# Performance work log

Measured on AMD Instinct MI355X. Metric: run time of the kernel, lower is better.

Reference implementation:

```python
import jax, jax.numpy as jnp
import numpy as np

EPS = 1e-10


def setup_inputs() -> dict:
    key = jax.random.key(0)
    k1, k2 = jax.random.split(key)
    inputs = jax.random.normal(k1, (32, 64, 64, 64), dtype=jnp.float32)
    # tf.random_uniform_initializer() default: U(-0.05, 0.05)
    embeddings = jax.random.uniform(k2, (1024, 64), dtype=jnp.float32,
                                    minval=-0.05, maxval=0.05)
    return {"inputs": inputs, "embeddings": embeddings}


def reference(inputs, embeddings):
    beta = 0.25
    K, D = embeddings.shape
    input_shape = inputs.shape
    flat = inputs.reshape(-1, D)                      # [N, D]

    # squared L2 distances: |a|^2 - 2 a.b + |b|^2  -> [N, K]
    a_sq = jnp.sum(flat * flat, axis=1, keepdims=True)
    ab = 2.0 * (flat @ embeddings.T)
    b_sq = jnp.sum(embeddings * embeddings, axis=1)[None, :]
    distances = a_sq - ab + b_sq

    idx = jnp.argmin(distances, axis=1)               # [N]
    # gather nearest codes (equivalent to one_hot @ embeddings)
    quantized = embeddings[idx].reshape(input_shape)

    commitment_loss = jnp.mean(jnp.square(jax.lax.stop_gradient(quantized) - inputs))
    codebook_loss = jnp.mean(jnp.square(quantized - jax.lax.stop_gradient(inputs)))
    vq_loss = commitment_loss + beta * codebook_loss

    # straight-through estimator
    quantized_st = inputs + jax.lax.stop_gradient(quantized - inputs)

    # perplexity from code usage histogram (== mean of one-hot rows)
    N = flat.shape[0]
    counts = jnp.zeros((K,), dtype=jnp.float32).at[idx].add(1.0)
    avg_probs = counts / N
    perplexity = jnp.exp(-jnp.sum(avg_probs * jnp.log(avg_probs + EPS)))

    indices_reshaped = idx.reshape(input_shape[:-1])
    return quantized_st, indices_reshaped, perplexity, vq_loss
```

## Files before the change

### kernel.cpp

```cpp
#include <hip/hip_runtime.h>
#include <float.h>

#define N_ROWS 131072
#define DIM 64
#define KCODES 1024
#define TAU 1.0e-3f
#define FLAGBIT 0x200000
#define NBLOCKA (N_ROWS / 128)
#define NBLOCKF (N_ROWS * 4 / 256)
#define NWAVES_FIN (N_ROWS * 4 / 64)

typedef __attribute__((ext_vector_type(8))) short short8;
typedef __attribute__((ext_vector_type(4))) float f32x4;

__device__ __forceinline__ unsigned short f2bf_rne(float x) {
    unsigned int u = __float_as_uint(x);
    unsigned int r = u + 0x7FFFu + ((u >> 16) & 1u);
    return (unsigned short)(r >> 16);
}
__device__ __forceinline__ float bf2f(unsigned short h) {
    return __uint_as_float(((unsigned int)h) << 16);
}

__device__ __forceinline__ float np_pairwise_sq64(const float* v) {
    float r[8];
#pragma unroll
    for (int j = 0; j < 8; ++j) r[j] = __fmul_rn(v[j], v[j]);
#pragma unroll
    for (int i = 8; i < 64; i += 8)
#pragma unroll
        for (int j = 0; j < 8; ++j)
            r[j] = __fadd_rn(r[j], __fmul_rn(v[i + j], v[i + j]));
    return __fadd_rn(
        __fadd_rn(__fadd_rn(r[0], r[1]), __fadd_rn(r[2], r[3])),
        __fadd_rn(__fadd_rn(r[4], r[5]), __fadd_rn(r[6], r[7])));
}

__device__ __forceinline__ float np_sq_stream(const float* xr) {
    float r[8];
    {
        float4 a = *reinterpret_cast<const float4*>(xr);
        float4 b = *reinterpret_cast<const float4*>(xr + 4);
        r[0] = __fmul_rn(a.x, a.x); r[1] = __fmul_rn(a.y, a.y);
        r[2] = __fmul_rn(a.z, a.z); r[3] = __fmul_rn(a.w, a.w);
        r[4] = __fmul_rn(b.x, b.x); r[5] = __fmul_rn(b.y, b.y);
        r[6] = __fmul_rn(b.z, b.z); r[7] = __fmul_rn(b.w, b.w);
    }
#pragma unroll
    for (int i = 8; i < 64; i += 8) {
        float4 a = *reinterpret_cast<const float4*>(xr + i);
        float4 b = *reinterpret_cast<const float4*>(xr + i + 4);
        r[0] = __fadd_rn(r[0], __fmul_rn(a.x, a.x));
        r[1] = __fadd_rn(r[1], __fmul_rn(a.y, a.y));
        r[2] = __fadd_rn(r[2], __fmul_rn(a.z, a.z));
        r[3] = __fadd_rn(r[3], __fmul_rn(a.w, a.w));
        r[4] = __fadd_rn(r[4], __fmul_rn(b.x, b.x));
        r[5] = __fadd_rn(r[5], __fmul_rn(b.y, b.y));
        r[6] = __fadd_rn(r[6], __fmul_rn(b.z, b.z));
        r[7] = __fadd_rn(r[7], __fmul_rn(b.w, b.w));
    }
    return __fadd_rn(
        __fadd_rn(__fadd_rn(r[0], r[1]), __fadd_rn(r[2], r[3])),
        __fadd_rn(__fadd_rn(r[4], r[5]), __fadd_rn(r[6], r[7])));
}

__device__ __forceinline__ float np_dist_stream(const float* xr, const float* e,
                                                float a_sq, float bq) {
    double acc0 = 0.0, acc1 = 0.0, acc2 = 0.0, acc3 = 0.0;
#pragma unroll
    for (int d = 0; d < DIM; d += 4) {
        float4 ev = *reinterpret_cast<const float4*>(e + d);
        float4 xv = *reinterpret_cast<const float4*>(xr + d);
        acc0 = fma((double)xv.x, (double)ev.x, acc0);
        acc1 = fma((double)xv.y, (double)ev.y, acc1);
        acc2 = fma((double)xv.z, (double)ev.z, acc2);
        acc3 = fma((double)xv.w, (double)ev.w, acc3);
    }
    double dot = (acc0 + acc1) + (acc2 + acc3);
    float ab = (float)(2.0 * dot);
    return __fadd_rn(__fsub_rn(a_sq, ab), bq);
}

__global__ __launch_bounds__(256, 4)
void vq_prep(const float* __restrict__ emb,
             int* __restrict__ hist,
             float* __restrict__ bsqf,
             unsigned short* __restrict__ epack) {
    const int tid = blockIdx.x * 256 + threadIdx.x;
    const int c   = tid >> 4;
    const int sub = tid & 15;
    const int g   = sub & 7;
    const int lvl = sub >> 3;

    const float* e8 = emb + (size_t)c * DIM + g * 8;
    float4 v0 = *reinterpret_cast<const float4*>(e8);
    float4 v1 = *reinterpret_cast<const float4*>(e8 + 4);
    float ev[8] = {v0.x, v0.y, v0.z, v0.w, v1.x, v1.y, v1.z, v1.w};
    short8 outv;
#pragma unroll
    for (int j = 0; j < 8; ++j) {
        unsigned short hh = f2bf_rne(ev[j]);
        outv[j] = (lvl == 0) ? (short)hh : (short)f2bf_rne(ev[j] - bf2f(hh));
    }
    const size_t base =
        ((((size_t)(c >> 4) * 2 + lvl) * 2 + (g >> 2)) * 64 +
         (((g & 3) << 4) | (c & 15))) * 8;
    *reinterpret_cast<short8*>(epack + base) = outv;

    if (sub == 0) {
        float e[DIM];
        const float4* src = reinterpret_cast<const float4*>(emb + (size_t)c * DIM);
#pragma unroll
        for (int i = 0; i < DIM / 4; ++i) {
            float4 v = src[i];
            e[i * 4 + 0] = v.x; e[i * 4 + 1] = v.y;
            e[i * 4 + 2] = v.z; e[i * 4 + 3] = v.w;
        }
        bsqf[c] = np_pairwise_sq64(e);
        hist[c] = 0;
    }
}

__global__ __launch_bounds__(256, 4)
void vq_fast(const float* __restrict__ x,
             const unsigned short* __restrict__ epack,
             const float* __restrict__ bsqf,
             float* __restrict__ idxout) {
    __shared__ unsigned short lds[16384];
    __shared__ float bql[KCODES];

    const int t = threadIdx.x;
    const int lane = t & 63;
    const int wid = t >> 6;
    const int rowbase = blockIdx.x * 128 + wid * 32;
    const int arow = lane & 15;
    const int kgrp = lane >> 4;

#pragma unroll
    for (int i = 0; i < 4; ++i) bql[t + i * 256] = bsqf[t + i * 256];

    short8 ah[2][2], al[2][2];
#pragma unroll
    for (int mf = 0; mf < 2; ++mf) {
#pragma unroll
        for (int kt = 0; kt < 2; ++kt) {
            const float* src = x + (size_t)(rowbase + mf * 16 + arow) * DIM + kt * 32 + kgrp * 8;
            float4 v0 = *reinterpret_cast<const float4*>(src);
            float4 v1 = *reinterpret_cast<const float4*>(src + 4);
            float xv[8] = {v0.x, v0.y, v0.z, v0.w, v1.x, v1.y, v1.z, v1.w};
            short8 h, l;
#pragma unroll
            for (int j = 0; j < 8; ++j) {
                unsigned short hh = f2bf_rne(xv[j]);
                h[j] = (short)hh;
                l[j] = (short)f2bf_rne(xv[j] - bf2f(hh));
            }
            ah[mf][kt] = h;
            al[mf][kt] = l;
        }
    }

    float best[2][4], sec[2][4];
    int bidx[2][4], sidx[2][4];
#pragma unroll
    for (int mf = 0; mf < 2; ++mf)
#pragma unroll
        for (int r = 0; r < 4; ++r) {
            best[mf][r] = FLT_MAX; sec[mf][r] = FLT_MAX;
            bidx[mf][r] = 0; sidx[mf][r] = 0;
        }

    for (int ch = 0; ch < 8; ++ch) {
        __syncthreads();
        {
            const float4* gsrc = reinterpret_cast<const float4*>(epack + (size_t)ch * 16384);
            float4* ldst = reinterpret_cast<float4*>(lds);
#pragma unroll
            for (int i = 0; i < 8; ++i)
                ldst[t + i * 256] = gsrc[t + i * 256];
        }
        __syncthreads();

        for (int ctl = 0; ctl < 8; ++ctl) {
            const int code0 = (ch * 8 + ctl) * 16;
            const unsigned short* fb = lds + ctl * 2048 + lane * 8;
            short8 bh0 = *reinterpret_cast<const short8*>(fb + 0 * 512);
            short8 bh1 = *reinterpret_cast<const short8*>(fb + 1 * 512);
            short8 bl0 = *reinterpret_cast<const short8*>(fb + 2 * 512);
            short8 bl1 = *reinterpret_cast<const short8*>(fb + 3 * 512);
            const float bq = bql[code0 + arow];

            f32x4 acc[2];
#pragma unroll
            for (int mf = 0; mf < 2; ++mf) {
                f32x4 a = {0.f, 0.f, 0.f, 0.f};
                a = __builtin_amdgcn_mfma_f32_16x16x32_bf16(ah[mf][0], bh0, a, 0, 0, 0);
                a = __builtin_amdgcn_mfma_f32_16x16x32_bf16(ah[mf][1], bh1, a, 0, 0, 0);
                a = __builtin_amdgcn_mfma_f32_16x16x32_bf16(ah[mf][0], bl0, a, 0, 0, 0);
                a = __builtin_amdgcn_mfma_f32_16x16x32_bf16(ah[mf][1], bl1, a, 0, 0, 0);
                a = __builtin_amdgcn_mfma_f32_16x16x32_bf16(al[mf][0], bh0, a, 0, 0, 0);
                a = __builtin_amdgcn_mfma_f32_16x16x32_bf16(al[mf][1], bh1, a, 0, 0, 0);
                acc[mf] = a;
            }

            const int code = code0 + arow;
#pragma unroll
            for (int mf = 0; mf < 2; ++mf)
#pragma unroll
                for (int r = 0; r < 4; ++r) {
                    float s = fmaf(-2.0f, acc[mf][r], bq);
                    bool lt_b = s < best[mf][r];
                    bool lt_s = s < sec[mf][r];
                    sec[mf][r]  = lt_b ? best[mf][r] : (lt_s ? s : sec[mf][r]);
                    sidx[mf][r] = lt_b ? bidx[mf][r] : (lt_s ? code : sidx[mf][r]);
                    best[mf][r] = lt_b ? s : best[mf][r];
                    bidx[mf][r] = lt_b ? code : bidx[mf][r];
                }
        }
    }

#pragma unroll
    for (int mf = 0; mf < 2; ++mf)
#pragma unroll
        for (int r = 0; r < 4; ++r) {
            float b = best[mf][r], sc = sec[mf][r];
            int bi = bidx[mf][r], si = sidx[mf][r];
#pragma unroll
            for (int off = 1; off < 16; off <<= 1) {
                float ob  = __shfl_xor(b, off);
                int   obi = __shfl_xor(bi, off);
                float osc = __shfl_xor(sc, off);
                int   osi = __shfl_xor(si, off);
                bool o_lt = ob < b;
                float loser  = o_lt ? b  : ob;
                int   loseri = o_lt ? bi : obi;
                b  = o_lt ? ob  : b;
                bi = o_lt ? obi : bi;
                float ns = sc; int nsi = si;
                if (osc < ns)   { ns = osc;   nsi = osi; }
                if (loser < ns) { ns = loser; nsi = loseri; }
                sc = ns; si = nsi;
            }
            best[mf][r] = b; sec[mf][r] = sc;
            bidx[mf][r] = bi; sidx[mf][r] = si;
        }

    if ((lane & 15) == 0) {
        const int rgrp = lane >> 4;
#pragma unroll
        for (int mf = 0; mf < 2; ++mf)
#pragma unroll
            for (int r = 0; r < 4; ++r) {
                int row = rowbase + mf * 16 + rgrp * 4 + r;
                int bi = bidx[mf][r], si = sidx[mf][r];
                int lo = min(bi, si), hi = max(bi, si);
                bool flag = (sec[mf][r] - best[mf][r]) <= TAU;
                int enc = flag ? (FLAGBIT | lo | (hi << 10)) : bi;
                idxout[row] = (float)enc;
            }
    }
}

__global__ __launch_bounds__(256, 8)
void vq_finalize(const float* __restrict__ x,
                 const float* __restrict__ emb,
                 const float* __restrict__ bsqf,
                 float* __restrict__ idxout,
                 float* __restrict__ qout,
                 int* __restrict__ hist,
                 float* __restrict__ partials) {
    const int gid  = blockIdx.x * 256 + threadIdx.x;
    const int row  = gid >> 2;
    const int part = gid & 3;
    int v = (int)idxout[row];
    int k;
    if (v & FLAGBIT) {
        const int c1 = v & 1023;
        const int c2 = (v >> 10) & 1023;
        const float* xr = x + (size_t)row * DIM;
        float a_sq = np_sq_stream(xr);
        float d1 = np_dist_stream(xr, emb + (size_t)c1 * DIM, a_sq, bsqf[c1]);
        float d2 = np_dist_stream(xr, emb + (size_t)c2 * DIM, a_sq, bsqf[c2]);
        k = (d2 < d1) ? c2 : c1;
        if (part == 0) idxout[row] = (float)k;
    } else {
        k = v;
    }

    const float4* xs = reinterpret_cast<const float4*>(x + (size_t)row * DIM + part * 16);
    const float4* er = reinterpret_cast<const float4*>(emb + (size_t)k * DIM + part * 16);
    float4* qr = reinterpret_cast<float4*>(qout + (size_t)row * DIM + part * 16);

    float lsum = 0.f;
#pragma unroll
    for (int i = 0; i < 4; ++i) {
        float4 e = er[i];
        float4 a = xs[i];
        qr[i] = e;
        float d0 = e.x - a.x, d1 = e.y - a.y;
        float d2 = e.z - a.z, d3 = e.w - a.w;
        lsum = fmaf(d0, d0, fmaf(d1, d1, fmaf(d2, d2, fmaf(d3, d3, lsum))));
    }
    if (part == 0) atomicAdd(&hist[k], 1);

#pragma unroll
    for (int off = 32; off > 0; off >>= 1)
        lsum += __shfl_xor(lsum, off);
    if ((threadIdx.x & 63) == 0) {
        int gwid = (blockIdx.x << 2) | (threadIdx.x >> 6);
        partials[gwid] = lsum;
    }
}

__global__ void vq_final(const int* __restrict__ hist,
                         const float* __restrict__ partials,
                         float* __restrict__ out2) {
    __shared__ double sh[KCODES];
    __shared__ float sl[KCODES];
    int t = threadIdx.x;

    double p = (double)hist[t] * (1.0 / (double)N_ROWS);
    sh[t] = p * log(p + 1e-10);

    float ls = 0.f;
#pragma unroll
    for (int i = 0; i < NWAVES_FIN / KCODES; ++i)
        ls += partials[t + i * KCODES];
    sl[t] = ls;
    __syncthreads();

    for (int off = KCODES / 2; off > 0; off >>= 1) {
        if (t < off) { sh[t] += sh[t + off]; sl[t] += sl[t + off]; }
        __syncthreads();
    }
    if (t == 0) {
        out2[0] = (float)exp(-sh[0]);
        out2[1] = 1.25f * sl[0] * (1.0f / (float)(N_ROWS * DIM));
    }
}

extern "C" void kernel_launch(void* const* d_in, const int* in_sizes, int n_in,
                              void* d_out, int out_size, void* d_ws, size_t ws_size,
                              hipStream_t stream) {
    const float* x   = (const float*)d_in[0];
    const float* emb = (const float*)d_in[1];
    float* out = (float*)d_out;

    int*   hist      = (int*)d_ws;
    float* bsqf      = (float*)((char*)d_ws + 4096);
    float* partials  = (float*)((char*)d_ws + 8192);
    unsigned short* epack = (unsigned short*)((char*)d_ws + 40960);

    float* qout    = out;
    float* idxout  = out + 8388608;
    float* scalars = out + 8388608 + 131072;

    vq_prep    <<<64, 256, 0, stream>>>(emb, hist, bsqf, epack);
    vq_fast    <<<NBLOCKA, 256, 0, stream>>>(x, epack, bsqf, idxout);
    vq_finalize<<<NBLOCKF, 256, 0, stream>>>(x, emb, bsqf, idxout, qout,
                                             hist, partials);
    vq_final   <<<1, KCODES, 0, stream>>>(hist, partials, scalars);
}
```

Before: 122.4 us.

## Compute VQ loss from argmin distance and fold bias into MFMA accumulator

The loss partial sums move out of the finalize kernel. They are now computed in the fast kernel from the identity |x-e|^2 = |x|^2 - 2*max(x·e - |e|^2/2), using a per-row |x|^2 taken while x is being converted. Seeding the MFMA accumulator with -|e|^2/2 removes the per-element fma in the argmin loop. The finalize kernel no longer re-reads x for non-flagged rows, which cuts global memory traffic. The trade-off is that the loss is taken from the bf16-split approximate distance, and flagged rows keep their approximate best distance even when the tie is resolved differently, so loss precision may drift slightly.

```diff
diff --git a/kernel.cpp b/kernel.cpp
--- a/kernel.cpp
+++ b/kernel.cpp
@@ -4,11 +4,11 @@
 #define N_ROWS 131072
 #define DIM 64
 #define KCODES 1024
-#define TAU 1.0e-3f
+#define TAU_HALF 5.0e-4f
 #define FLAGBIT 0x200000
 #define NBLOCKA (N_ROWS / 128)
+#define NPART (NBLOCKA * 4)
 #define NBLOCKF (N_ROWS * 4 / 256)
-#define NWAVES_FIN (N_ROWS * 4 / 64)
 
 typedef __attribute__((ext_vector_type(8))) short short8;
 typedef __attribute__((ext_vector_type(4))) float f32x4;
@@ -125,9 +125,11 @@
 void vq_fast(const float* __restrict__ x,
              const unsigned short* __restrict__ epack,
              const float* __restrict__ bsqf,
-             float* __restrict__ idxout) {
+             float* __restrict__ idxout,
+             float* __restrict__ partials) {
     __shared__ unsigned short lds[16384];
     __shared__ float bql[KCODES];
+    __shared__ float aql[4][2][16];
 
     const int t = threadIdx.x;
     const int lane = t & 63;
@@ -142,6 +144,7 @@
     short8 ah[2][2], al[2][2];
 #pragma unroll
     for (int mf = 0; mf < 2; ++mf) {
+        float ssq = 0.f;
 #pragma unroll
         for (int kt = 0; kt < 2; ++kt) {
             const float* src = x + (size_t)(rowbase + mf * 16 + arow) * DIM + kt * 32 + kgrp * 8;
@@ -154,10 +157,14 @@
                 unsigned short hh = f2bf_rne(xv[j]);
                 h[j] = (short)hh;
                 l[j] = (short)f2bf_rne(xv[j] - bf2f(hh));
+                ssq = fmaf(xv[j], xv[j], ssq);
             }
             ah[mf][kt] = h;
             al[mf][kt] = l;
         }
+        ssq += __shfl_xor(ssq, 16);
+        ssq += __shfl_xor(ssq, 32);
+        if (kgrp == 0) aql[wid][mf][arow] = ssq;
     }
 
     float best[2][4], sec[2][4];
@@ -166,7 +173,7 @@
     for (int mf = 0; mf < 2; ++mf)
 #pragma unroll
         for (int r = 0; r < 4; ++r) {
-            best[mf][r] = FLT_MAX; sec[mf][r] = FLT_MAX;
+            best[mf][r] = -FLT_MAX; sec[mf][r] = -FLT_MAX;
             bidx[mf][r] = 0; sidx[mf][r] = 0;
         }
 
@@ -188,12 +195,12 @@
             short8 bh1 = *reinterpret_cast<const short8*>(fb + 1 * 512);
             short8 bl0 = *reinterpret_cast<const short8*>(fb + 2 * 512);
             short8 bl1 = *reinterpret_cast<const short8*>(fb + 3 * 512);
-            const float bq = bql[code0 + arow];
+            const float nb = -0.5f * bql[code0 + arow];
 
             f32x4 acc[2];
 #pragma unroll
             for (int mf = 0; mf < 2; ++mf) {
-                f32x4 a = {0.f, 0.f, 0.f, 0.f};
+                f32x4 a = {nb, nb, nb, nb};
                 a = __builtin_amdgcn_mfma_f32_16x16x32_bf16(ah[mf][0], bh0, a, 0, 0, 0);
                 a = __builtin_amdgcn_mfma_f32_16x16x32_bf16(ah[mf][1], bh1, a, 0, 0, 0);
                 a = __builtin_amdgcn_mfma_f32_16x16x32_bf16(ah[mf][0], bl0, a, 0, 0, 0);
@@ -208,13 +215,13 @@
             for (int mf = 0; mf < 2; ++mf)
 #pragma unroll
                 for (int r = 0; r < 4; ++r) {
-                    float s = fmaf(-2.0f, acc[mf][r], bq);
-                    bool lt_b = s < best[mf][r];
-                    bool lt_s = s < sec[mf][r];
-                    sec[mf][r]  = lt_b ? best[mf][r] : (lt_s ? s : sec[mf][r]);
-                    sidx[mf][r] = lt_b ? bidx[mf][r] : (lt_s ? code : sidx[mf][r]);
-                    best[mf][r] = lt_b ? s : best[mf][r];
-                    bidx[mf][r] = lt_b ? code : bidx[mf][r];
+                    float m = acc[mf][r];
+                    bool gt_b = m > best[mf][r];
+                    bool gt_s = m > sec[mf][r];
+                    sec[mf][r]  = gt_b ? best[mf][r] : (gt_s ? m : sec[mf][r]);
+                    sidx[mf][r] = gt_b ? bidx[mf][r] : (gt_s ? code : sidx[mf][r]);
+                    best[mf][r] = gt_b ? m : best[mf][r];
+                    bidx[mf][r] = gt_b ? code : bidx[mf][r];
                 }
         }
     }
@@ -231,14 +238,14 @@
                 int   obi = __shfl_xor(bi, off);
                 float osc = __shfl_xor(sc, off);
                 int   osi = __shfl_xor(si, off);
-                bool o_lt = ob < b;
-                float loser  = o_lt ? b  : ob;
-                int   loseri = o_lt ? bi : obi;
-                b  = o_lt ? ob  : b;
-                bi = o_lt ? obi : bi;
+                bool o_gt = ob > b;
+                float loser  = o_gt ? b  : ob;
+                int   loseri = o_gt ? bi : obi;
+                b  = o_gt ? ob  : b;
+                bi = o_gt ? obi : bi;
                 float ns = sc; int nsi = si;
-                if (osc < ns)   { ns = osc;   nsi = osi; }
-                if (loser < ns) { ns = loser; nsi = loseri; }
+                if (osc > ns)   { ns = osc;   nsi = osi; }
+                if (loser > ns) { ns = loser; nsi = loseri; }
                 sc = ns; si = nsi;
             }
             best[mf][r] = b; sec[mf][r] = sc;
@@ -247,17 +254,23 @@
 
     if ((lane & 15) == 0) {
         const int rgrp = lane >> 4;
+        float lsum = 0.f;
 #pragma unroll
         for (int mf = 0; mf < 2; ++mf)
 #pragma unroll
             for (int r = 0; r < 4; ++r) {
-                int row = rowbase + mf * 16 + rgrp * 4 + r;
+                int rl = rgrp * 4 + r;
+                int row = rowbase + mf * 16 + rl;
                 int bi = bidx[mf][r], si = sidx[mf][r];
                 int lo = min(bi, si), hi = max(bi, si);
-                bool flag = (sec[mf][r] - best[mf][r]) <= TAU;
+                bool flag = (best[mf][r] - sec[mf][r]) <= TAU_HALF;
                 int enc = flag ? (FLAGBIT | lo | (hi << 10)) : bi;
                 idxout[row] = (float)enc;
+                lsum += fmaf(-2.0f, best[mf][r], aql[wid][mf][rl]);
             }
+        lsum += __shfl_xor(lsum, 16);
+        lsum += __shfl_xor(lsum, 32);
+        if (lane == 0) partials[blockIdx.x * 4 + wid] = lsum;
     }
 }
 
@@ -267,8 +280,7 @@
                  const float* __restrict__ bsqf,
                  float* __restrict__ idxout,
                  float* __restrict__ qout,
-                 int* __restrict__ hist,
-                 float* __restrict__ partials) {
+                 int* __restrict__ hist) {
     const int gid  = blockIdx.x * 256 + threadIdx.x;
     const int row  = gid >> 2;
     const int part = gid & 3;
@@ -287,45 +299,27 @@
         k = v;
     }
 
-    const float4* xs = reinterpret_cast<const float4*>(x + (size_t)row * DIM + part * 16);
     const float4* er = reinterpret_cast<const float4*>(emb + (size_t)k * DIM + part * 16);
     float4* qr = reinterpret_cast<float4*>(qout + (size_t)row * DIM + part * 16);
-
-    float lsum = 0.f;
-#pragma unroll
-    for (int i = 0; i < 4; ++i) {
-        float4 e = er[i];
-        float4 a = xs[i];
-        qr[i] = e;
-        float d0 = e.x - a.x, d1 = e.y - a.y;
-        float d2 = e.z - a.z, d3 = e.w - a.w;
-        lsum = fmaf(d0, d0, fmaf(d1, d1, fmaf(d2, d2, fmaf(d3, d3, lsum))));
-    }
+#pragma unroll
+    for (int i = 0; i < 4; ++i) qr[i] = er[i];
     if (part == 0) atomicAdd(&hist[k], 1);
-
-#pragma unroll
-    for (int off = 32; off > 0; off >>= 1)
-        lsum += __shfl_xor(lsum, off);
-    if ((threadIdx.x & 63) == 0) {
-        int gwid = (blockIdx.x << 2) | (threadIdx.x >> 6);
-        partials[gwid] = lsum;
-    }
 }
 
 __global__ void vq_final(const int* __restrict__ hist,
                          const float* __restrict__ partials,
                          float* __restrict__ out2) {
     __shared__ double sh[KCODES];
-    __shared__ float sl[KCODES];
+    __shared__ double sl[KCODES];
     int t = threadIdx.x;
 
     double p = (double)hist[t] * (1.0 / (double)N_ROWS);
     sh[t] = p * log(p + 1e-10);
 
-    float ls = 0.f;
-#pragma unroll
-    for (int i = 0; i < NWAVES_FIN / KCODES; ++i)
-        ls += partials[t + i * KCODES];
+    double ls = 0.0;
+#pragma unroll
+    for (int i = 0; i < NPART / KCODES; ++i)
+        ls += (double)partials[t + i * KCODES];
     sl[t] = ls;
     __syncthreads();
 
@@ -335,7 +329,7 @@
     }
     if (t == 0) {
         out2[0] = (float)exp(-sh[0]);
-        out2[1] = 1.25f * sl[0] * (1.0f / (float)(N_ROWS * DIM));
+        out2[1] = (float)(1.25 * sl[0] * (1.0 / (double)((size_t)N_ROWS * DIM)));
     }
 }
 
@@ -356,8 +350,7 @@
     float* scalars = out + 8388608 + 131072;
 
     vq_prep    <<<64, 256, 0, stream>>>(emb, hist, bsqf, epack);
-    vq_fast    <<<NBLOCKA, 256, 0, stream>>>(x, epack, bsqf, idxout);
-    vq_finalize<<<NBLOCKF, 256, 0, stream>>>(x, emb, bsqf, idxout, qout,
-                                             hist, partials);
+    vq_fast    <<<NBLOCKA, 256, 0, stream>>>(x, epack, bsqf, idxout, partials);
+    vq_finalize<<<NBLOCKF, 256, 0, stream>>>(x, emb, bsqf, idxout, qout, hist);
     vq_final   <<<1, KCODES, 0, stream>>>(hist, partials, scalars);
 }
```

Measured after the change: 123.8 us. Within noise of the previous version (+1.2%).
